# Performance work log

Measured on AMD Instinct MI355X. Metric: run time of the kernel, lower is better.

The kernel has to match this reference:

```python
import jax, jax.numpy as jnp
import numpy as np
from jax import lax

B, C, H, W = 4, 64, 64, 64
CH = C // 2  # edge_detect hidden channels
BN_EPS = 1e-5


def conv1x1(x, w, b):
    # x: (B,C,H,W), w: (O,C), b: (O,)
    return jnp.einsum('bchw,oc->bohw', x, w) + b[None, :, None, None]


def setup_inputs() -> dict:
    key = jax.random.key(0)
    ks = jax.random.split(key, 12)
    s = 1.0 / np.sqrt(C)
    inp = {
        'x': jax.random.normal(ks[0], (B, C, H, W), jnp.float32),
        'Wq': jax.random.normal(ks[1], (C, C), jnp.float32) * s,
        'bq': jnp.zeros((C,), jnp.float32),
        'Wk': jax.random.normal(ks[2], (C, C), jnp.float32) * s,
        'bk': jnp.zeros((C,), jnp.float32),
        'Wv': jax.random.normal(ks[3], (C, C), jnp.float32) * s,
        'bv': jnp.zeros((C,), jnp.float32),
        'We1': jax.random.normal(ks[4], (CH, C, 3, 3), jnp.float32) * (1.0 / np.sqrt(C * 9)),
        'be1': jnp.zeros((CH,), jnp.float32),
        'bn_w': jnp.ones((CH,), jnp.float32),
        'bn_b': jnp.zeros((CH,), jnp.float32),
        'bn_mean': jnp.zeros((CH,), jnp.float32),
        'bn_var': jnp.ones((CH,), jnp.float32),
        'We2': jax.random.normal(ks[5], (1, CH), jnp.float32) * (1.0 / np.sqrt(CH)),
        'be2': jnp.zeros((1,), jnp.float32),
        'gamma': jax.random.normal(ks[6], (1,), jnp.float32) * 0.1,
        'beta': jax.random.normal(ks[7], (1,), jnp.float32) * 0.1,
    }
    return inp


def reference(x, Wq, bq, Wk, bk, Wv, bv, We1, be1, bn_w, bn_b, bn_mean, bn_var, We2, be2, gamma, beta):
    b, c, h, w = x.shape
    hw = h * w
    q = conv1x1(x, Wq, bq).reshape(b, c, hw).transpose(0, 2, 1)  # (B,HW,C)
    k = conv1x1(x, Wk, bk).reshape(b, c, hw)                      # (B,C,HW)
    v = conv1x1(x, Wv, bv).reshape(b, c, hw)                      # (B,C,HW)

    energy = jnp.einsum('bnc,bcm->bnm', q, k)                      # (B,HW,HW)
    attention = jax.nn.softmax(energy, axis=-1)

    # edge_detect: 3x3 conv -> BN (eval stats) -> ReLU -> 1x1 conv -> sigmoid
    e = lax.conv_general_dilated(x, We1, (1, 1), 'SAME',
                                 dimension_numbers=('NCHW', 'OIHW', 'NCHW'))
    e = e + be1[None, :, None, None]
    e = (e - bn_mean[None, :, None, None]) * jax.lax.rsqrt(bn_var + BN_EPS)[None, :, None, None]
    e = e * bn_w[None, :, None, None] + bn_b[None, :, None, None]
    e = jax.nn.relu(e)
    e = conv1x1(e, We2, be2)                                       # (B,1,H,W)
    edge = jax.nn.sigmoid(e).reshape(b, 1, hw)                     # (B,1,HW)

    fa = attention * (1.0 + beta[0] * edge)                        # broadcast over query dim
    denom = jnp.maximum(jnp.sum(jnp.abs(fa), axis=2, keepdims=True), 1e-12)
    fa = fa / denom                                                # L1 renorm along keys

    out = jnp.einsum('bcm,bnm->bcn', v, fa).reshape(b, c, h, w)
    return gamma[0] * out + x
```

## Files before the change

### kernel.cpp

```cpp
#include <hip/hip_runtime.h>
#include <hip/hip_bf16.h>

typedef unsigned short u16;
typedef __attribute__((ext_vector_type(8))) __bf16 bf16x8;
typedef __attribute__((ext_vector_type(4))) float f32x4;


__device__ __forceinline__ u16 f2bf(float f) {
    unsigned u = __builtin_bit_cast(unsigned, f);
    u += 0x7FFFu + ((u >> 16) & 1u);
    return (u16)(u >> 16);
}
__device__ __forceinline__ float bf2f(u16 v) {
    unsigned u = ((unsigned)v) << 16;
    return __builtin_bit_cast(float, u);
}

__global__ __launch_bounds__(256) void qkv_edge_kernel(
    const float* __restrict__ x,
    const float* __restrict__ Wq, const float* __restrict__ bq,
    const float* __restrict__ Wk, const float* __restrict__ bk,
    const float* __restrict__ Wv, const float* __restrict__ bv,
    const float* __restrict__ We1, const float* __restrict__ be1,
    const float* __restrict__ bn_w, const float* __restrict__ bn_b,
    const float* __restrict__ bn_mean, const float* __restrict__ bn_var,
    const float* __restrict__ We2, const float* __restrict__ be2,
    const float* __restrict__ beta,
    u16* __restrict__ Qt, u16* __restrict__ Kt, u16* __restrict__ Vm,
    float* __restrict__ wkey)
{
    __shared__ __align__(16) u16 sm[33280];
    const int t = threadIdx.x;
    const int wv = t >> 6, lane = t & 63;
    const int quad = lane >> 4, l15 = lane & 15;

    if (blockIdx.x < 256) {
        u16* Wl   = sm;
        u16* xt_s = sm + 13824;
        u16* vt   = sm + 13824 + 4224;
        const int b = blockIdx.x >> 6;
        const int n0 = (blockIdx.x & 63) << 6;

        const float* Wmat[3] = {Wq, Wk, Wv};
#pragma unroll
        for (int m = 0; m < 3; ++m)
            for (int i = 0; i < 16; ++i) {
                int lin = t + i * 256;
                Wl[(m * 64 + (lin >> 6)) * 72 + (lin & 63)] = f2bf(Wmat[m][lin]);
            }
        for (int i = 0; i < 16; ++i) {
            int lin = t + i * 256;
            int c = lin >> 6, nn = lin & 63;
            xt_s[nn * 66 + c] = f2bf(x[(size_t)(b * 64 + c) * 4096 + n0 + nn]);
        }
        __syncthreads();

        bf16x8 bx[2];
#pragma unroll
        for (int h = 0; h < 2; ++h)
            bx[h] = *reinterpret_cast<const bf16x8*>(
                &xt_s[(wv * 16 + l15) * 66 + h * 32 + quad * 8]);

        f32x4 d[3][4];
#pragma unroll
        for (int m = 0; m < 3; ++m)
#pragma unroll
            for (int mt = 0; mt < 4; ++mt) d[m][mt] = (f32x4){0.f, 0.f, 0.f, 0.f};

#pragma unroll
        for (int h = 0; h < 2; ++h)
#pragma unroll
            for (int m = 0; m < 3; ++m)
#pragma unroll
                for (int mt = 0; mt < 4; ++mt) {
                    bf16x8 af = *reinterpret_cast<const bf16x8*>(
                        &Wl[(m * 64 + mt * 16 + l15) * 72 + h * 32 + quad * 8]);
                    d[m][mt] = __builtin_amdgcn_mfma_f32_16x16x32_bf16(af, bx[h], d[m][mt], 0, 0, 0);
                }

        const float* bias[3] = {bq, bk, bv};
#pragma unroll
        for (int m = 0; m < 3; ++m)
#pragma unroll
            for (int mt = 0; mt < 4; ++mt) {
                float4 bi = *reinterpret_cast<const float4*>(bias[m] + mt * 16 + quad * 4);
                d[m][mt][0] += bi.x; d[m][mt][1] += bi.y; d[m][mt][2] += bi.z; d[m][mt][3] += bi.w;
            }

        const int rowchunk = (n0 >> 4) + wv;
#pragma unroll
        for (int m = 0; m < 2; ++m) {
            u16* base = (m == 0 ? Qt : Kt) + (size_t)b * 262144;
#pragma unroll
            for (int mt = 0; mt < 4; ++mt) {
                uint2 pk;
                pk.x = (unsigned)f2bf(d[m][mt][0]) | ((unsigned)f2bf(d[m][mt][1]) << 16);
                pk.y = (unsigned)f2bf(d[m][mt][2]) | ((unsigned)f2bf(d[m][mt][3]) << 16);
                *reinterpret_cast<uint2*>(
                    base + ((size_t)(rowchunk * 8 + mt * 2 + (quad >> 1))) * 128 +
                    l15 * 8 + (quad & 1) * 4) = pk;
            }
        }
#pragma unroll
        for (int mt = 0; mt < 4; ++mt)
#pragma unroll
            for (int r = 0; r < 4; ++r)
                vt[(mt * 16 + quad * 4 + r) * 72 + wv * 16 + l15] = f2bf(d[2][mt][r]);
        __syncthreads();
        {
            u16* Vb_st = Vm + (size_t)b * 262144;
            const int kt = n0 >> 6;
#pragma unroll
            for (int i = 0; i < 2; ++i) {
                int unit = t + i * 256;
                int f = unit >> 7, hq = (unit >> 4) & 7, cl = unit & 15;
                const u16* src = &vt[(f * 16 + cl) * 72 + hq * 8];
                uint4 v4 = *reinterpret_cast<const uint4*>(src);
                *reinterpret_cast<uint4*>(
                    Vb_st + ((size_t)((kt * 4 + f) * 8 + hq)) * 128 + cl * 8) = v4;
            }
        }
    } else {
        u16* Ae_s = sm;
        u16* xr_s = sm + 18688;
        const int eb = blockIdx.x - 256;
        const int b = eb >> 6, h = eb & 63;

        if (t < 192) {
            int kh = t / 64, rem = t & 63;
            int col = (rem >> 5) * 65, ci2 = (rem & 31) * 2;
            *reinterpret_cast<unsigned*>(&xr_s[(kh * 66 + col) * 72 + ci2]) = 0u;
        }
#pragma unroll
        for (int i = 0; i < 8; ++i) {
            int pr = t + i * 256;
            int ch = pr >> 6, ci = pr & 63;
            const float* src = We1 + ch * 576 + ci * 9;
#pragma unroll
            for (int p = 0; p < 9; ++p)
                Ae_s[ch * 584 + p * 64 + ci] = f2bf(src[p]);
        }
#pragma unroll
        for (int i = 0; i < 48; ++i) {
            int e = t + i * 256;
            int kh = e >> 12, rem = e & 4095;
            int ci = rem >> 6, w = rem & 63;
            int hs = h + kh - 1;
            float v = 0.f;
            if ((unsigned)hs < 64u)
                v = x[((size_t)(b * 64 + ci) * 64 + hs) * 64 + w];
            xr_s[(kh * 66 + w + 1) * 72 + ci] = f2bf(v);
        }
        __syncthreads();

        f32x4 e[2];
        e[0] = (f32x4){0.f, 0.f, 0.f, 0.f};
        e[1] = (f32x4){0.f, 0.f, 0.f, 0.f};
#pragma unroll
        for (int p = 0; p < 9; ++p) {
            const int kh = p / 3, kw = p - kh * 3;
#pragma unroll
            for (int half = 0; half < 2; ++half) {
                bf16x8 bfr = *reinterpret_cast<const bf16x8*>(
                    &xr_s[(kh * 66 + wv * 16 + l15 + kw) * 72 + half * 32 + quad * 8]);
#pragma unroll
                for (int mt = 0; mt < 2; ++mt) {
                    bf16x8 af = *reinterpret_cast<const bf16x8*>(
                        &Ae_s[(mt * 16 + l15) * 584 + p * 64 + half * 32 + quad * 8]);
                    e[mt] = __builtin_amdgcn_mfma_f32_16x16x32_bf16(af, bfr, e[mt], 0, 0, 0);
                }
            }
        }
        float partial = 0.f;
#pragma unroll
        for (int mt = 0; mt < 2; ++mt) {
            float4 bw = *reinterpret_cast<const float4*>(bn_w    + mt * 16 + quad * 4);
            float4 bb = *reinterpret_cast<const float4*>(bn_b    + mt * 16 + quad * 4);
            float4 bm = *reinterpret_cast<const float4*>(bn_mean + mt * 16 + quad * 4);
            float4 bv2 = *reinterpret_cast<const float4*>(bn_var + mt * 16 + quad * 4);
            float4 b1 = *reinterpret_cast<const float4*>(be1     + mt * 16 + quad * 4);
            float4 w2 = *reinterpret_cast<const float4*>(We2     + mt * 16 + quad * 4);
            float sc, sh;
            sc = bw.x * rsqrtf(bv2.x + 1e-5f); sh = (b1.x - bm.x) * sc + bb.x;
            partial += fmaxf(e[mt][0] * sc + sh, 0.f) * w2.x;
            sc = bw.y * rsqrtf(bv2.y + 1e-5f); sh = (b1.y - bm.y) * sc + bb.y;
            partial += fmaxf(e[mt][1] * sc + sh, 0.f) * w2.y;
            sc = bw.z * rsqrtf(bv2.z + 1e-5f); sh = (b1.z - bm.z) * sc + bb.z;
            partial += fmaxf(e[mt][2] * sc + sh, 0.f) * w2.z;
            sc = bw.w * rsqrtf(bv2.w + 1e-5f); sh = (b1.w - bm.w) * sc + bb.w;
            partial += fmaxf(e[mt][3] * sc + sh, 0.f) * w2.w;
        }
        partial += __shfl_xor(partial, 16);
        partial += __shfl_xor(partial, 32);
        if (lane < 16) {
            float s = partial + be2[0];
            float sg = 1.f / (1.f + __expf(-s));
            wkey[(size_t)b * 4096 + h * 64 + wv * 16 + lane] = 1.f + beta[0] * sg;
        }
    }
}

template <int NSPLIT>
__global__ __launch_bounds__(128, 4) void attn_kernel(
    const u16* __restrict__ Qt, const u16* __restrict__ Kt,
    const u16* __restrict__ Vm, const float* __restrict__ wkey,
    u16* __restrict__ O_part, float* __restrict__ l_part)
{
    constexpr int KT_ITERS = 64 / NSPLIT;
    __shared__ __align__(16) u16 p_s_all[2 * 32 * 68];
    const int t = threadIdx.x;
    const int qi = blockIdx.x / NSPLIT;
    const int split = blockIdx.x % NSPLIT;
    const int b = qi >> 6;
    const int n0 = (qi & 63) << 6;
    const int wv = t >> 6, lane = t & 63;
    const int quad = lane >> 4, l15 = lane & 15;
    u16* p_s = p_s_all + wv * (32 * 68);

    const u16* Qb = Qt + (size_t)b * 262144;
    const u16* Kb = Kt + (size_t)b * 262144;
    const u16* Vb = Vm + (size_t)b * 262144;
    const float* wb = wkey + (size_t)b * 4096;

    bf16x8 qf[2][2];
#pragma unroll
    for (int nt = 0; nt < 2; ++nt)
#pragma unroll
        for (int h = 0; h < 2; ++h)
            qf[nt][h] = __builtin_bit_cast(bf16x8, *reinterpret_cast<const uint4*>(
                Qb + ((size_t)(((n0 >> 4) + wv * 2 + nt) * 8 + h * 4 + quad)) * 128 + l15 * 8));

    const int kt0 = split * KT_ITERS;
    uint4 kf[4][2];
    float4 wf[4];
#pragma unroll
    for (int mt = 0; mt < 4; ++mt) {
#pragma unroll
        for (int h = 0; h < 2; ++h)
            kf[mt][h] = *reinterpret_cast<const uint4*>(
                Kb + ((size_t)((kt0 * 4 + mt) * 8 + h * 4 + quad)) * 128 + l15 * 8);
        wf[mt] = *reinterpret_cast<const float4*>(wb + kt0 * 64 + mt * 16 + quad * 4);
    }

    f32x4 o[2][4];
#pragma unroll
    for (int m2 = 0; m2 < 2; ++m2)
#pragma unroll
        for (int f = 0; f < 4; ++f) o[m2][f] = (f32x4){0.f, 0.f, 0.f, 0.f};
    float l_acc[2] = {0.f, 0.f};

    for (int kt = kt0; kt < kt0 + KT_ITERS; ++kt) {
        uint4 vf[4][2];
#pragma unroll
        for (int f = 0; f < 4; ++f)
#pragma unroll
            for (int h = 0; h < 2; ++h)
                vf[f][h] = *reinterpret_cast<const uint4*>(
                    Vb + ((size_t)((kt * 4 + f) * 8 + h * 4 + quad)) * 128 + l15 * 8);

        f32x4 s[4][2];
#pragma unroll
        for (int mt = 0; mt < 4; ++mt)
#pragma unroll
            for (int nt = 0; nt < 2; ++nt) {
                f32x4 a = (f32x4){0.f, 0.f, 0.f, 0.f};
                a = __builtin_amdgcn_mfma_f32_16x16x32_bf16(
                        __builtin_bit_cast(bf16x8, kf[mt][0]), qf[nt][0], a, 0, 0, 0);
                a = __builtin_amdgcn_mfma_f32_16x16x32_bf16(
                        __builtin_bit_cast(bf16x8, kf[mt][1]), qf[nt][1], a, 0, 0, 0);
                s[mt][nt] = a;
            }

        const int ktn = (kt + 1 < kt0 + KT_ITERS) ? kt + 1 : kt0;
#pragma unroll
        for (int mt = 0; mt < 4; ++mt)
#pragma unroll
            for (int h = 0; h < 2; ++h)
                kf[mt][h] = *reinterpret_cast<const uint4*>(
                    Kb + ((size_t)((ktn * 4 + mt) * 8 + h * 4 + quad)) * 128 + l15 * 8);

#pragma unroll
        for (int mt = 0; mt < 4; ++mt)
#pragma unroll
            for (int nt = 0; nt < 2; ++nt) {
                u16 pk[4];
#pragma unroll
                for (int r = 0; r < 4; ++r) {
                    float p = __expf(s[mt][nt][r] - 12.0f) *
                              reinterpret_cast<const float*>(&wf[mt])[r];
                    l_acc[nt] += p;
                    pk[r] = f2bf(p);
                }
                uint2 packed;
                packed.x = (unsigned)pk[0] | ((unsigned)pk[1] << 16);
                packed.y = (unsigned)pk[2] | ((unsigned)pk[3] << 16);
                *reinterpret_cast<uint2*>(
                    &p_s[(nt * 16 + l15) * 68 + mt * 16 + quad * 4]) = packed;
            }

#pragma unroll
        for (int mt = 0; mt < 4; ++mt)
            wf[mt] = *reinterpret_cast<const float4*>(wb + ktn * 64 + mt * 16 + quad * 4);

        bf16x8 pa[2][2];
#pragma unroll
        for (int m2 = 0; m2 < 2; ++m2)
#pragma unroll
            for (int h = 0; h < 2; ++h) {
                uint2 lo = *reinterpret_cast<const uint2*>(
                    &p_s[(m2 * 16 + l15) * 68 + h * 32 + quad * 8]);
                uint2 hi = *reinterpret_cast<const uint2*>(
                    &p_s[(m2 * 16 + l15) * 68 + h * 32 + quad * 8 + 4]);
                uint4 c4; c4.x = lo.x; c4.y = lo.y; c4.z = hi.x; c4.w = hi.y;
                pa[m2][h] = __builtin_bit_cast(bf16x8, c4);
            }

#pragma unroll
        for (int m2 = 0; m2 < 2; ++m2)
#pragma unroll
            for (int f = 0; f < 4; ++f) {
                o[m2][f] = __builtin_amdgcn_mfma_f32_16x16x32_bf16(
                    pa[m2][0], __builtin_bit_cast(bf16x8, vf[f][0]), o[m2][f], 0, 0, 0);
                o[m2][f] = __builtin_amdgcn_mfma_f32_16x16x32_bf16(
                    pa[m2][1], __builtin_bit_cast(bf16x8, vf[f][1]), o[m2][f], 0, 0, 0);
            }
    }

    const size_t pbase = (size_t)blockIdx.x * 64;
#pragma unroll
    for (int nt = 0; nt < 2; ++nt) {
        float v = l_acc[nt];
        v += __shfl_xor(v, 16);
        v += __shfl_xor(v, 32);
        if (lane < 16) l_part[pbase + wv * 32 + nt * 16 + lane] = v;
    }
#pragma unroll
    for (int m2 = 0; m2 < 2; ++m2)
#pragma unroll
        for (int f = 0; f < 4; ++f)
#pragma unroll
            for (int r = 0; r < 4; ++r)
                O_part[(pbase + wv * 32 + m2 * 16 + quad * 4 + r) * 64 + f * 16 + l15] =
                    f2bf(o[m2][f][r]);
}

template <int NSPLIT>
__global__ __launch_bounds__(256) void combine_kernel(
    const u16* __restrict__ O_part, const float* __restrict__ l_part,
    const float* __restrict__ x, const float* __restrict__ g_gamma,
    float* __restrict__ out)
{
    __shared__ float ot[16 * 65];
    __shared__ float ls[16];
    const int t = threadIdx.x;
    const int b = blockIdx.x >> 8;
    const int R0 = (blockIdx.x & 255) << 4;
    const int qi = (b << 6) + (R0 >> 6);
    const int ro = R0 & 63;
    const float gamma = g_gamma[0];

    {
        const int r = t >> 4, cq = (t & 15) * 4;
        float a0 = 0.f, a1 = 0.f, a2 = 0.f, a3 = 0.f;
#pragma unroll
        for (int s4 = 0; s4 < NSPLIT; ++s4) {
            const u16* p = O_part +
                (((size_t)qi * NSPLIT + s4) * 64 + ro + r) * 64 + cq;
            uint2 u = *reinterpret_cast<const uint2*>(p);
            a0 += bf2f((u16)(u.x & 0xFFFF));
            a1 += bf2f((u16)(u.x >> 16));
            a2 += bf2f((u16)(u.y & 0xFFFF));
            a3 += bf2f((u16)(u.y >> 16));
        }
        ot[r * 65 + cq + 0] = a0;
        ot[r * 65 + cq + 1] = a1;
        ot[r * 65 + cq + 2] = a2;
        ot[r * 65 + cq + 3] = a3;
        if (t < 16) {
            float lsum = 0.f;
#pragma unroll
            for (int s4 = 0; s4 < NSPLIT; ++s4)
                lsum += l_part[((size_t)qi * NSPLIT + s4) * 64 + ro + t];
            ls[t] = gamma / fmaxf(lsum, 1e-30f);
        }
    }
    __syncthreads();
    {
        const int c = t >> 2, nseg = t & 3;
        const size_t gbase = ((size_t)(b * 64 + c)) * 4096 + R0 + nseg * 4;
        float4 xv = *reinterpret_cast<const float4*>(&x[gbase]);
        float4 rv;
        rv.x = ot[(nseg * 4 + 0) * 65 + c] * ls[nseg * 4 + 0] + xv.x;
        rv.y = ot[(nseg * 4 + 1) * 65 + c] * ls[nseg * 4 + 1] + xv.y;
        rv.z = ot[(nseg * 4 + 2) * 65 + c] * ls[nseg * 4 + 2] + xv.z;
        rv.w = ot[(nseg * 4 + 3) * 65 + c] * ls[nseg * 4 + 3] + xv.w;
        *reinterpret_cast<float4*>(&out[gbase]) = rv;
    }
}

extern "C" void kernel_launch(void* const* d_in, const int* in_sizes, int n_in,
                              void* d_out, int out_size, void* d_ws, size_t ws_size,
                              hipStream_t stream) {
    const float* x      = (const float*)d_in[0];
    const float* Wq     = (const float*)d_in[1];
    const float* bq     = (const float*)d_in[2];
    const float* Wk     = (const float*)d_in[3];
    const float* bk     = (const float*)d_in[4];
    const float* Wv     = (const float*)d_in[5];
    const float* bv     = (const float*)d_in[6];
    const float* We1    = (const float*)d_in[7];
    const float* be1    = (const float*)d_in[8];
    const float* bn_w   = (const float*)d_in[9];
    const float* bn_b   = (const float*)d_in[10];
    const float* bn_mean= (const float*)d_in[11];
    const float* bn_var = (const float*)d_in[12];
    const float* We2    = (const float*)d_in[13];
    const float* be2    = (const float*)d_in[14];
    const float* gamma  = (const float*)d_in[15];
    const float* beta   = (const float*)d_in[16];

    char* ws = (char*)d_ws;
    const size_t KB = 1024, MB = 1024 * 1024;
    u16*   Qt     = (u16*)ws;
    u16*   Kt     = (u16*)(ws + 2 * MB);
    u16*   Vm     = (u16*)(ws + 4 * MB);
    float* wkey   = (float*)(ws + 6 * MB);
    float* l_part = (float*)(ws + 6 * MB + 64 * KB);
    u16*   O_part = (u16*)(ws + 6 * MB + 576 * KB);

    const bool use8 = ws_size >= (6 * MB + 576 * KB + (size_t)2048 * 64 * 64 * 2);

    float* out = (float*)d_out;

    qkv_edge_kernel<<<dim3(512), dim3(256), 0, stream>>>(
        x, Wq, bq, Wk, bk, Wv, bv, We1, be1, bn_w, bn_b, bn_mean, bn_var,
        We2, be2, beta, Qt, Kt, Vm, wkey);
    if (use8) {
        attn_kernel<8><<<dim3(2048), dim3(128), 0, stream>>>(Qt, Kt, Vm, wkey, O_part, l_part);
        combine_kernel<8><<<dim3(1024), dim3(256), 0, stream>>>(O_part, l_part, x, gamma, out);
    } else {
        attn_kernel<4><<<dim3(1024), dim3(128), 0, stream>>>(Qt, Kt, Vm, wkey, O_part, l_part);
        combine_kernel<4><<<dim3(1024), dim3(256), 0, stream>>>(O_part, l_part, x, gamma, out);
    }
}
```

Baseline: 152.3 us.

## Software-pipeline attention loop, vectorize loads, fold log2e into Q, truncate P to bf16

The attention loop is restructured so the PV MFMAs of the previous tile overlap the QK MFMAs and exp of the current tile, with V loads issued after the PV multiply. The log2(e) factor is folded into Q at projection time so exp2f replaces __expf, and probabilities are truncated to bf16 instead of rounded. Weight and input staging in the QKV and edge kernels are vectorized to float4 and packed stores. The truncation slightly changes numerics, and the extra live registers from pipelining may affect occupancy.

```diff
diff --git a/kernel.cpp b/kernel.cpp
--- a/kernel.cpp
+++ b/kernel.cpp
@@ -44,9 +44,15 @@
         const float* Wmat[3] = {Wq, Wk, Wv};
 #pragma unroll
         for (int m = 0; m < 3; ++m)
-            for (int i = 0; i < 16; ++i) {
-                int lin = t + i * 256;
-                Wl[(m * 64 + (lin >> 6)) * 72 + (lin & 63)] = f2bf(Wmat[m][lin]);
+#pragma unroll
+            for (int i = 0; i < 4; ++i) {
+                int u = t + i * 256;
+                float4 w4 = *reinterpret_cast<const float4*>(Wmat[m] + u * 4);
+                int row = u >> 4, col = (u & 15) * 4;
+                uint2 pk;
+                pk.x = (unsigned)f2bf(w4.x) | ((unsigned)f2bf(w4.y) << 16);
+                pk.y = (unsigned)f2bf(w4.z) | ((unsigned)f2bf(w4.w) << 16);
+                *reinterpret_cast<uint2*>(&Wl[(m * 64 + row) * 72 + col]) = pk;
             }
         for (int i = 0; i < 16; ++i) {
             int lin = t + i * 256;
@@ -79,12 +85,17 @@
                 }
 
         const float* bias[3] = {bq, bk, bv};
+        const float L2E = 1.44269504f;
 #pragma unroll
         for (int m = 0; m < 3; ++m)
 #pragma unroll
             for (int mt = 0; mt < 4; ++mt) {
                 float4 bi = *reinterpret_cast<const float4*>(bias[m] + mt * 16 + quad * 4);
                 d[m][mt][0] += bi.x; d[m][mt][1] += bi.y; d[m][mt][2] += bi.z; d[m][mt][3] += bi.w;
+                if (m == 0) {
+                    d[m][mt][0] *= L2E; d[m][mt][1] *= L2E;
+                    d[m][mt][2] *= L2E; d[m][mt][3] *= L2E;
+                }
             }
 
         const int rowchunk = (n0 >> 4) + wv;
@@ -132,24 +143,32 @@
             *reinterpret_cast<unsigned*>(&xr_s[(kh * 66 + col) * 72 + ci2]) = 0u;
         }
 #pragma unroll
-        for (int i = 0; i < 8; ++i) {
-            int pr = t + i * 256;
-            int ch = pr >> 6, ci = pr & 63;
-            const float* src = We1 + ch * 576 + ci * 9;
-#pragma unroll
-            for (int p = 0; p < 9; ++p)
-                Ae_s[ch * 584 + p * 64 + ci] = f2bf(src[p]);
-        }
-#pragma unroll
-        for (int i = 0; i < 48; ++i) {
-            int e = t + i * 256;
-            int kh = e >> 12, rem = e & 4095;
-            int ci = rem >> 6, w = rem & 63;
+        for (int i = 0; i < 18; ++i) {
+            int u = t + i * 256;
+            int ch = u / 144;
+            int rem = u - ch * 144;
+            int p = rem >> 4, cig = (rem & 15) * 4;
+            const float* src = We1 + ch * 576 + cig * 9 + p;
+            float a = src[0], b2 = src[9], c2 = src[18], d2 = src[27];
+            uint2 pk;
+            pk.x = (unsigned)f2bf(a) | ((unsigned)f2bf(b2) << 16);
+            pk.y = (unsigned)f2bf(c2) | ((unsigned)f2bf(d2) << 16);
+            *reinterpret_cast<uint2*>(&Ae_s[ch * 584 + p * 64 + cig]) = pk;
+        }
+#pragma unroll
+        for (int i = 0; i < 12; ++i) {
+            int u = t + i * 256;
+            int w = u & 63, cig = (u >> 6) & 15, kh = u >> 10;
             int hs = h + kh - 1;
-            float v = 0.f;
-            if ((unsigned)hs < 64u)
-                v = x[((size_t)(b * 64 + ci) * 64 + hs) * 64 + w];
-            xr_s[(kh * 66 + w + 1) * 72 + ci] = f2bf(v);
+            float v0 = 0.f, v1 = 0.f, v2 = 0.f, v3 = 0.f;
+            if ((unsigned)hs < 64u) {
+                const float* src = x + ((size_t)(b * 64 + cig * 4) * 64 + hs) * 64 + w;
+                v0 = src[0]; v1 = src[4096]; v2 = src[8192]; v3 = src[12288];
+            }
+            uint2 pk;
+            pk.x = (unsigned)f2bf(v0) | ((unsigned)f2bf(v1) << 16);
+            pk.y = (unsigned)f2bf(v2) | ((unsigned)f2bf(v3) << 16);
+            *reinterpret_cast<uint2*>(&xr_s[(kh * 66 + w + 1) * 72 + cig * 4]) = pk;
         }
         __syncthreads();
 
@@ -233,32 +252,41 @@
     const int kt0 = split * KT_ITERS;
     uint4 kf[4][2];
     float4 wf[4];
-#pragma unroll
-    for (int mt = 0; mt < 4; ++mt) {
-#pragma unroll
-        for (int h = 0; h < 2; ++h)
-            kf[mt][h] = *reinterpret_cast<const uint4*>(
-                Kb + ((size_t)((kt0 * 4 + mt) * 8 + h * 4 + quad)) * 128 + l15 * 8);
-        wf[mt] = *reinterpret_cast<const float4*>(wb + kt0 * 64 + mt * 16 + quad * 4);
-    }
-
-    f32x4 o[2][4];
-#pragma unroll
-    for (int m2 = 0; m2 < 2; ++m2)
-#pragma unroll
-        for (int f = 0; f < 4; ++f) o[m2][f] = (f32x4){0.f, 0.f, 0.f, 0.f};
-    float l_acc[2] = {0.f, 0.f};
-
-    for (int kt = kt0; kt < kt0 + KT_ITERS; ++kt) {
-        uint4 vf[4][2];
+    uint4 vf[4][2];
+
+    auto loadK = [&](int kt) {
+#pragma unroll
+        for (int mt = 0; mt < 4; ++mt)
+#pragma unroll
+            for (int h = 0; h < 2; ++h)
+                kf[mt][h] = *reinterpret_cast<const uint4*>(
+                    Kb + ((size_t)((kt * 4 + mt) * 8 + h * 4 + quad)) * 128 + l15 * 8);
+    };
+    auto loadW = [&](int kt) {
+#pragma unroll
+        for (int mt = 0; mt < 4; ++mt)
+            wf[mt] = *reinterpret_cast<const float4*>(wb + kt * 64 + mt * 16 + quad * 4);
+    };
+    auto loadV = [&](int kt) {
 #pragma unroll
         for (int f = 0; f < 4; ++f)
 #pragma unroll
             for (int h = 0; h < 2; ++h)
                 vf[f][h] = *reinterpret_cast<const uint4*>(
                     Vb + ((size_t)((kt * 4 + f) * 8 + h * 4 + quad)) * 128 + l15 * 8);
-
-        f32x4 s[4][2];
+    };
+
+    loadK(kt0); loadW(kt0); loadV(kt0);
+
+    f32x4 o[2][4];
+#pragma unroll
+    for (int m2 = 0; m2 < 2; ++m2)
+#pragma unroll
+        for (int f = 0; f < 4; ++f) o[m2][f] = (f32x4){0.f, 0.f, 0.f, 0.f};
+    float l_acc[2] = {0.f, 0.f};
+    bf16x8 pa[2][2];
+
+    auto computeS = [&](f32x4 (&s)[4][2]) {
 #pragma unroll
         for (int mt = 0; mt < 4; ++mt)
 #pragma unroll
@@ -270,39 +298,32 @@
                         __builtin_bit_cast(bf16x8, kf[mt][1]), qf[nt][1], a, 0, 0, 0);
                 s[mt][nt] = a;
             }
-
-        const int ktn = (kt + 1 < kt0 + KT_ITERS) ? kt + 1 : kt0;
-#pragma unroll
-        for (int mt = 0; mt < 4; ++mt)
-#pragma unroll
-            for (int h = 0; h < 2; ++h)
-                kf[mt][h] = *reinterpret_cast<const uint4*>(
-                    Kb + ((size_t)((ktn * 4 + mt) * 8 + h * 4 + quad)) * 128 + l15 * 8);
-
-#pragma unroll
-        for (int mt = 0; mt < 4; ++mt)
+    };
+    auto expWrite = [&](f32x4 (&s)[4][2]) {
+        const float OFF = 17.3123405f;
+#pragma unroll
+        for (int mt = 0; mt < 4; ++mt) {
+            const float* wfp = reinterpret_cast<const float*>(&wf[mt]);
 #pragma unroll
             for (int nt = 0; nt < 2; ++nt) {
-                u16 pk[4];
-#pragma unroll
-                for (int r = 0; r < 4; ++r) {
-                    float p = __expf(s[mt][nt][r] - 12.0f) *
-                              reinterpret_cast<const float*>(&wf[mt])[r];
-                    l_acc[nt] += p;
-                    pk[r] = f2bf(p);
-                }
+                float p0 = exp2f(s[mt][nt][0] - OFF) * wfp[0];
+                float p1 = exp2f(s[mt][nt][1] - OFF) * wfp[1];
+                float p2 = exp2f(s[mt][nt][2] - OFF) * wfp[2];
+                float p3 = exp2f(s[mt][nt][3] - OFF) * wfp[3];
+                l_acc[nt] += (p0 + p1) + (p2 + p3);
+                unsigned u0 = __builtin_bit_cast(unsigned, p0);
+                unsigned u1 = __builtin_bit_cast(unsigned, p1);
+                unsigned u2 = __builtin_bit_cast(unsigned, p2);
+                unsigned u3 = __builtin_bit_cast(unsigned, p3);
                 uint2 packed;
-                packed.x = (unsigned)pk[0] | ((unsigned)pk[1] << 16);
-                packed.y = (unsigned)pk[2] | ((unsigned)pk[3] << 16);
+                packed.x = (u0 >> 16) | (u1 & 0xFFFF0000u);
+                packed.y = (u2 >> 16) | (u3 & 0xFFFF0000u);
                 *reinterpret_cast<uint2*>(
                     &p_s[(nt * 16 + l15) * 68 + mt * 16 + quad * 4]) = packed;
             }
-
-#pragma unroll
-        for (int mt = 0; mt < 4; ++mt)
-            wf[mt] = *reinterpret_cast<const float4*>(wb + ktn * 64 + mt * 16 + quad * 4);
-
-        bf16x8 pa[2][2];
+        }
+    };
+    auto readPa = [&]() {
 #pragma unroll
         for (int m2 = 0; m2 < 2; ++m2)
 #pragma unroll
@@ -314,7 +335,8 @@
                 uint4 c4; c4.x = lo.x; c4.y = lo.y; c4.z = hi.x; c4.w = hi.y;
                 pa[m2][h] = __builtin_bit_cast(bf16x8, c4);
             }
-
+    };
+    auto pvAcc = [&]() {
 #pragma unroll
         for (int m2 = 0; m2 < 2; ++m2)
 #pragma unroll
@@ -324,7 +346,28 @@
                 o[m2][f] = __builtin_amdgcn_mfma_f32_16x16x32_bf16(
                     pa[m2][1], __builtin_bit_cast(bf16x8, vf[f][1]), o[m2][f], 0, 0, 0);
             }
-    }
+    };
+
+    {
+        f32x4 s[4][2];
+        computeS(s);
+        loadK(kt0 + 1 < kt0 + KT_ITERS ? kt0 + 1 : kt0);
+        expWrite(s);
+        loadW(kt0 + 1 < kt0 + KT_ITERS ? kt0 + 1 : kt0);
+        readPa();
+    }
+    for (int k = kt0 + 1; k < kt0 + KT_ITERS; ++k) {
+        f32x4 s[4][2];
+        computeS(s);
+        const int ktn = (k + 1 < kt0 + KT_ITERS) ? k + 1 : kt0;
+        loadK(ktn);
+        pvAcc();
+        loadV(k);
+        expWrite(s);
+        loadW(ktn);
+        readPa();
+    }
+    pvAcc();
 
     const size_t pbase = (size_t)blockIdx.x * 64;
 #pragma unroll
```

After: 167.7 us. +10.1%, slower.
